# Optimization experiments

Measured on AMD Instinct MI355X. Metric: run time of the kernel, lower is better.

## Reference

```python
import jax, jax.numpy as jnp
import numpy as np

B, N, E, H = 2, 256, 768, 12
D = E // H
LOG_2PI = float(np.log(2.0 * np.pi))


def setup_inputs() -> dict:
    key = jax.random.key(0)
    ks = jax.random.split(key, 8)
    return {
        "x": jax.random.normal(ks[0], (B, N, E), jnp.float32),
        "Wqkv": jax.random.normal(ks[1], (E, 3 * E), jnp.float32) * 0.02,
        "bqkv": jax.random.normal(ks[2], (3 * E,), jnp.float32) * 0.02,
        "Wproj": jax.random.normal(ks[3], (E, E), jnp.float32) * 0.02,
        "bproj": jax.random.normal(ks[4], (E,), jnp.float32) * 0.02,
        "mean": jax.random.normal(ks[5], (E, E), jnp.float32),
        "logvar": jax.random.normal(ks[6], (E, E), jnp.float32),
        "mix_coef": jax.random.normal(ks[7], (E,), jnp.float32),
    }


def reference(x, Wqkv, bqkv, Wproj, bproj, mean, logvar, mix_coef):
    b, n, e = x.shape
    # qkv projection; einops 'b n (h d qkv) -> qkv b h n d' (qkv is the INNERMOST split)
    qkv = (x @ Wqkv + bqkv).reshape(b, n, H, D, 3)
    qkv = jnp.transpose(qkv, (4, 0, 2, 1, 3))  # (3, b, h, n, d)
    q, k, v = qkv[0], qkv[1], qkv[2]

    # keys back to (b, n, e): 'b h n d -> b n (h d)'
    keys = jnp.transpose(k, (0, 2, 1, 3)).reshape(b, n, e)

    # MixtureSameFamily.log_prob: component Normal batch (E, E), mixture over last dim.
    # out[b,n,i] = logsumexp_j( log_softmax(mix_coef)[j] + logN(keys[b,n,i]; mean[i,j], std[i,j]) )
    log_mix = jax.nn.log_softmax(mix_coef)                      # (E,)
    std = jnp.exp(0.5 * logvar)                                  # (E, E)
    z = (keys[:, :, :, None] - mean[None, None, :, :]) / std     # (b, n, E, E)
    comp_lp = -0.5 * (z * z) - jnp.log(std) - 0.5 * LOG_2PI      # (b, n, E, E)
    key_mix = jax.nn.logsumexp(comp_lp + log_mix, axis=-1)       # (b, n, E)

    # 'b n (h d) -> b h n d'
    key_mix = jnp.transpose(key_mix.reshape(b, n, H, D), (0, 2, 1, 3))

    energy = jnp.einsum("bhqd,bhkd->bhqk", q, key_mix)
    att = jax.nn.softmax(energy, axis=-1) / jnp.sqrt(jnp.float32(e))
    out = jnp.einsum("bhql,bhld->bhqd", att, v)                  # (b, h, n, d)
    out = jnp.transpose(out, (0, 2, 1, 3)).reshape(b, n, e)
    return out @ Wproj + bproj
```

## Files before the change

### kernel.cpp

```cpp
#include <hip/hip_runtime.h>

#define LOG2E 1.4426950408889634f
#define LN2 0.6931471805599453f

typedef __attribute__((ext_vector_type(8))) short bf16x8;
typedef __attribute__((ext_vector_type(4))) float f32x4;
typedef __attribute__((ext_vector_type(2))) float f32x2;

constexpr int Ee = 768;
constexpr int BN = 512;
constexpr long QC_OFF = 0;
constexpr long KT_OFF = 393216;
constexpr long VC_OFF = 786432;
constexpr long KM_OFF = 1179648;
constexpr long EN_OFF = 1572864;
constexpr long OA_OFF = 3145728;

__device__ __forceinline__ unsigned pk_hi(float x0, float x1) {
    return (__float_as_uint(x0) >> 16) | (__float_as_uint(x1) & 0xFFFF0000u);
}
__device__ __forceinline__ float rhi(float x) {
    return __uint_as_float(__float_as_uint(x) & 0xFFFF0000u);
}
__device__ __forceinline__ f32x2 pk_fma2(f32x2 a, f32x2 b, f32x2 c) {
    f32x2 d;
    asm("v_pk_fma_f32 %0, %1, %2, %3" : "=v"(d) : "v"(a), "v"(b), "v"(c));
    return d;
}
__device__ __forceinline__ f32x2 pk_add2(f32x2 a, f32x2 b) {
    f32x2 d;
    asm("v_pk_add_f32 %0, %1, %2" : "=v"(d) : "v"(a), "v"(b));
    return d;
}

template<int EPI>
__global__ __launch_bounds__(256)
void mfma_gemm(const float* __restrict__ A, int lda, long sAb, long sAh,
               const float* __restrict__ Bm, int ldb, long sBb, long sBh,
               float* __restrict__ C, int ldc, long sCb, long sCh,
               const float* __restrict__ bias, int K, int Hdiv,
               float* __restrict__ eq, float* __restrict__ ek,
               float* __restrict__ ev)
{
    __shared__ __align__(16) unsigned short sm[4 * 64 * 64];
    char* const smb = (char*)sm;
    const int tid = threadIdx.x;
    const int m0 = blockIdx.x * 64, n0 = blockIdx.y * 64;
    const int zb = blockIdx.z / Hdiv, zh = blockIdx.z - zb * Hdiv;
    A  += zb * sAb + zh * sAh;
    Bm += zb * sBb + zh * sBh;
    C  += zb * sCb + zh * sCh;

    const int lane = tid & 63, w = tid >> 6;
    const int wr = w >> 1, wc = w & 1;
    const int fr = lane & 15, fko2 = (lane >> 4) * 16;

    const bool isB = tid < 128;
    const int kq = isB ? (tid >> 4) : ((tid - 128) & 7);
    const int nq = tid & 15;
    const int mq = (tid - 128) >> 3;

    auto foff = [](int plane, int row, int cb) {
        return plane * 8192 + row * 128 + (cb ^ ((row & 7) << 4));
    };
    int wo[8];
    if (isB) {
        #pragma unroll
        for (int e = 0; e < 4; ++e) {
            wo[e]     = foff(2, nq * 4 + e, kq * 8);
            wo[e + 4] = foff(3, nq * 4 + e, kq * 8);
        }
    } else {
        #pragma unroll
        for (int r = 0; r < 4; ++r) {
            wo[r]     = foff(0, mq * 4 + r, kq * 8);
            wo[r + 4] = foff(1, mq * 4 + r, kq * 8);
        }
    }
    const int oA0h = foff(0, wr * 32 + fr,      fko2);
    const int oA1h = foff(0, wr * 32 + 16 + fr, fko2);
    const int oA0l = oA0h + 8192, oA1l = oA1h + 8192;
    const int oB0h = foff(2, wc * 32 + fr,      fko2);
    const int oB1h = foff(2, wc * 32 + 16 + fr, fko2);
    const int oB0l = oB0h + 8192, oB1l = oB1h + 8192;

    f32x4 acc00 = {}, acc01 = {}, acc10 = {}, acc11 = {};
    float4 r0, r1, r2, r3;

    auto load_regs = [&](int k0) {
        if (isB) {
            const float* p = &Bm[(long)(k0 + kq * 4) * ldb + n0 + nq * 4];
            r0 = *(const float4*)p; p += ldb;
            r1 = *(const float4*)p; p += ldb;
            r2 = *(const float4*)p; p += ldb;
            r3 = *(const float4*)p;
        } else {
            const float* p = &A[(long)(m0 + mq * 4) * lda + k0 + kq * 4];
            r0 = *(const float4*)p; p += lda;
            r1 = *(const float4*)p; p += lda;
            r2 = *(const float4*)p; p += lda;
            r3 = *(const float4*)p;
        }
    };

    auto cvt_store = [&](const float4& v, int o_hi, int o_lo) {
        uint2 hi; hi.x = pk_hi(v.x, v.y); hi.y = pk_hi(v.z, v.w);
        const float l0 = v.x - rhi(v.x), l1 = v.y - rhi(v.y);
        const float l2 = v.z - rhi(v.z), l3 = v.w - rhi(v.w);
        uint2 lo; lo.x = pk_hi(l0, l1); lo.y = pk_hi(l2, l3);
        *(uint2*)(smb + o_hi) = hi;
        *(uint2*)(smb + o_lo) = lo;
    };

    auto stage = [&]() {
        if (isB) {
            #pragma unroll
            for (int e = 0; e < 4; ++e) {
                float4 col;
                col.x = (&r0.x)[e]; col.y = (&r1.x)[e];
                col.z = (&r2.x)[e]; col.w = (&r3.x)[e];
                cvt_store(col, wo[e], wo[e + 4]);
            }
        } else {
            cvt_store(r0, wo[0], wo[4]);
            cvt_store(r1, wo[1], wo[5]);
            cvt_store(r2, wo[2], wo[6]);
            cvt_store(r3, wo[3], wo[7]);
        }
    };

    load_regs(0);
    for (int k0 = 0; k0 < K; k0 += 32) {
        __syncthreads();
        stage();
        __syncthreads();
        if (k0 + 32 < K) load_regs(k0 + 32);
        const bf16x8 Ah0 = *(const bf16x8*)(smb + oA0h);
        const bf16x8 Ah1 = *(const bf16x8*)(smb + oA1h);
        const bf16x8 Al0 = *(const bf16x8*)(smb + oA0l);
        const bf16x8 Al1 = *(const bf16x8*)(smb + oA1l);
        const bf16x8 Bh0 = *(const bf16x8*)(smb + oB0h);
        const bf16x8 Bh1 = *(const bf16x8*)(smb + oB1h);
        const bf16x8 Bl0 = *(const bf16x8*)(smb + oB0l);
        const bf16x8 Bl1 = *(const bf16x8*)(smb + oB1l);
        acc00 = __builtin_amdgcn_mfma_f32_16x16x32_bf16(Ah0, Bh0, acc00, 0, 0, 0);
        acc01 = __builtin_amdgcn_mfma_f32_16x16x32_bf16(Ah0, Bh1, acc01, 0, 0, 0);
        acc10 = __builtin_amdgcn_mfma_f32_16x16x32_bf16(Ah1, Bh0, acc10, 0, 0, 0);
        acc11 = __builtin_amdgcn_mfma_f32_16x16x32_bf16(Ah1, Bh1, acc11, 0, 0, 0);
        acc00 = __builtin_amdgcn_mfma_f32_16x16x32_bf16(Ah0, Bl0, acc00, 0, 0, 0);
        acc01 = __builtin_amdgcn_mfma_f32_16x16x32_bf16(Ah0, Bl1, acc01, 0, 0, 0);
        acc10 = __builtin_amdgcn_mfma_f32_16x16x32_bf16(Ah1, Bl0, acc10, 0, 0, 0);
        acc11 = __builtin_amdgcn_mfma_f32_16x16x32_bf16(Ah1, Bl1, acc11, 0, 0, 0);
        acc00 = __builtin_amdgcn_mfma_f32_16x16x32_bf16(Al0, Bh0, acc00, 0, 0, 0);
        acc01 = __builtin_amdgcn_mfma_f32_16x16x32_bf16(Al0, Bh1, acc01, 0, 0, 0);
        acc10 = __builtin_amdgcn_mfma_f32_16x16x32_bf16(Al1, Bh0, acc10, 0, 0, 0);
        acc11 = __builtin_amdgcn_mfma_f32_16x16x32_bf16(Al1, Bh1, acc11, 0, 0, 0);
    }

    const int rb = m0 + wr * 32 + (lane >> 4) * 4;
    const int cb = n0 + wc * 32 + fr;
    if (EPI == 1) {
        auto scat = [&](int row, int col, float x) {
            x += bias[col];
            const int i = col / 3, s = col - i * 3;
            if (s == 0)      eq[(long)row * Ee + i] = x;
            else if (s == 1) ek[(long)i * BN + row] = x;
            else             ev[(long)row * Ee + i] = x;
        };
        #pragma unroll
        for (int j = 0; j < 4; ++j) {
            scat(rb + j,      cb,      acc00[j]);
            scat(rb + j,      cb + 16, acc01[j]);
            scat(rb + j + 16, cb,      acc10[j]);
            scat(rb + j + 16, cb + 16, acc11[j]);
        }
    } else {
        const float b0  = bias ? bias[cb]      : 0.f;
        const float b16 = bias ? bias[cb + 16] : 0.f;
        #pragma unroll
        for (int j = 0; j < 4; ++j) C[(long)(rb + j +  0) * ldc + cb +  0] = acc00[j] + b0;
        #pragma unroll
        for (int j = 0; j < 4; ++j) C[(long)(rb + j +  0) * ldc + cb + 16] = acc01[j] + b16;
        #pragma unroll
        for (int j = 0; j < 4; ++j) C[(long)(rb + j + 16) * ldc + cb +  0] = acc10[j] + b0;
        #pragma unroll
        for (int j = 0; j < 4; ++j) C[(long)(rb + j + 16) * ldc + cb + 16] = acc11[j] + b16;
    }
}

__global__ __launch_bounds__(512)
void k_mixture(const float* __restrict__ mean, const float* __restrict__ logvar,
               const float* __restrict__ mix, const float* __restrict__ keysT,
               float* __restrict__ kmT)
{
    __shared__ __align__(16) float aS[768], bS[768], cS[768];
    __shared__ float sP[512][9];
    const int i = blockIdx.x;
    const int tid = threadIdx.x;

    for (int j = tid; j < 768; j += 512) {
        const float lv = logvar[i * Ee + j];
        const float mu = mean[i * Ee + j];
        const float istd2 = __builtin_amdgcn_exp2f(-lv * LOG2E);
        aS[j] = -0.5f * LOG2E * istd2;
        bS[j] = LOG2E * mu * istd2;
        cS[j] = fmaf(-0.5f * LOG2E * mu * mu, istd2, LOG2E * (mix[j] - 0.5f * lv));
    }
    __syncthreads();

    const int rg = tid & 63;
    const int jg = tid >> 6;
    f32x2 kvd[8], k2d[8], s2[8];
    #pragma unroll
    for (int q = 0; q < 8; ++q) {
        const float kv = keysT[(long)i * BN + q * 64 + rg];
        const float k2 = kv * kv;
        kvd[q] = (f32x2){kv, kv};
        k2d[q] = (f32x2){k2, k2};
        s2[q] = (f32x2){0.f, 0.f};
    }
    const float4* a4 = (const float4*)(aS + jg * 96);
    const float4* b4 = (const float4*)(bS + jg * 96);
    const float4* c4 = (const float4*)(cS + jg * 96);
    for (int it = 0; it < 24; ++it) {
        const float4 a = a4[it], b = b4[it], c = c4[it];
        const f32x2 a01 = {a.x, a.y}, a23 = {a.z, a.w};
        const f32x2 b01 = {b.x, b.y}, b23 = {b.z, b.w};
        const f32x2 c01 = {c.x, c.y}, c23 = {c.z, c.w};
        #pragma unroll
        for (int q = 0; q < 8; ++q) {
            f32x2 t0 = pk_fma2(a01, k2d[q], pk_fma2(b01, kvd[q], c01));
            f32x2 t1 = pk_fma2(a23, k2d[q], pk_fma2(b23, kvd[q], c23));
            f32x2 e0 = { __builtin_amdgcn_exp2f(t0.x), __builtin_amdgcn_exp2f(t0.y) };
            f32x2 e1 = { __builtin_amdgcn_exp2f(t1.x), __builtin_amdgcn_exp2f(t1.y) };
            s2[q] = pk_add2(s2[q], e0);
            s2[q] = pk_add2(s2[q], e1);
        }
    }
    #pragma unroll
    for (int q = 0; q < 8; ++q)
        sP[q * 64 + rg][jg] = s2[q].x + s2[q].y;
    __syncthreads();

    const float* rp = sP[tid];
    const float t0 = ((rp[0] + rp[1]) + (rp[2] + rp[3]))
                   + ((rp[4] + rp[5]) + (rp[6] + rp[7]));
    kmT[(long)i * BN + tid] = LN2 * __builtin_amdgcn_logf(t0);
}

__global__ __launch_bounds__(256)
void k_smpv(const float* __restrict__ energy, const float* __restrict__ vc,
            float* __restrict__ oat)
{
    __shared__ __align__(16) unsigned short att[32768];
    __shared__ __align__(16) unsigned short bv[8192];
    char* const attb = (char*)att;
    char* const bvb  = (char*)bv;
    const int tid = threadIdx.x;
    const int tile = blockIdx.x, bh = blockIdx.y;
    const int b = bh / 12, h = bh - b * 12;
    const float* E = energy + (long)bh * 65536 + (long)tile * 64 * 256;
    const float* V = vc + (long)b * 196608 + h * 64;
    float* O = oat + ((long)b * 256 + tile * 64) * 768 + h * 64;

    const int w = tid >> 6, lane = tid & 63;

    {
        const int rl = w * 16 + (lane >> 2);
        const int mq = (lane & 3) * 64;
        float4 ev[16];
        const float* erow = E + (long)rl * 256 + mq;
        #pragma unroll
        for (int t = 0; t < 16; ++t) ev[t] = *(const float4*)(erow + t * 4);
        float mx = -__builtin_inff();
        #pragma unroll
        for (int t = 0; t < 16; ++t)
            mx = fmaxf(mx, fmaxf(fmaxf(ev[t].x, ev[t].y), fmaxf(ev[t].z, ev[t].w)));
        mx = fmaxf(mx, __shfl_xor(mx, 1, 64));
        mx = fmaxf(mx, __shfl_xor(mx, 2, 64));
        float sum = 0.f;
        #pragma unroll
        for (int t = 0; t < 16; ++t) {
            ev[t].x = __builtin_amdgcn_exp2f((ev[t].x - mx) * LOG2E);
            ev[t].y = __builtin_amdgcn_exp2f((ev[t].y - mx) * LOG2E);
            ev[t].z = __builtin_amdgcn_exp2f((ev[t].z - mx) * LOG2E);
            ev[t].w = __builtin_amdgcn_exp2f((ev[t].w - mx) * LOG2E);
            sum += (ev[t].x + ev[t].y) + (ev[t].z + ev[t].w);
        }
        sum += __shfl_xor(sum, 1, 64);
        sum += __shfl_xor(sum, 2, 64);
        const float sc = 1.0f / (sum * 27.712812921102035f);
        const int rxor = (rl & 7) << 4;
        #pragma unroll
        for (int t = 0; t < 16; ++t) {
            const float x0 = ev[t].x * sc, x1 = ev[t].y * sc;
            const float x2 = ev[t].z * sc, x3 = ev[t].w * sc;
            uint2 hi; hi.x = pk_hi(x0, x1); hi.y = pk_hi(x2, x3);
            const float l0 = x0 - rhi(x0), l1 = x1 - rhi(x1);
            const float l2 = x2 - rhi(x2), l3 = x3 - rhi(x3);
            uint2 lo; lo.x = pk_hi(l0, l1); lo.y = pk_hi(l2, l3);
            const int cb = (mq + t * 4) * 2;
            *(uint2*)(attb + (long)rl * 512 + (cb ^ rxor))         = hi;
            *(uint2*)(attb + 32768 + (long)rl * 512 + (cb ^ rxor)) = lo;
        }
    }

    const int wr = w >> 1, wc = w & 1;
    const int fr = lane & 15, fko2 = (lane >> 4) * 16;
    const int rA0 = wr * 32 + fr, rA1 = rA0 + 16;
    const int rB0 = wc * 32 + fr, rB1 = rB0 + 16;
    const int xA0 = (rA0 & 7) << 4, xA1 = (rA1 & 7) << 4;
    const int oB0h = rB0 * 128 + (fko2 ^ ((rB0 & 7) << 4));
    const int oB1h = rB1 * 128 + (fko2 ^ ((rB1 & 7) << 4));
    const int oB0l = oB0h + 8192, oB1l = oB1h + 8192;

    const bool isB = tid < 128;
    const int kq = tid >> 4;
    const int nq = tid & 15;
    int wo[8];
    #pragma unroll
    for (int e = 0; e < 4; ++e) {
        const int row = nq * 4 + e;
        wo[e]     = row * 128 + ((kq * 8) ^ ((row & 7) << 4));
        wo[e + 4] = wo[e] + 8192;
    }

    f32x4 acc00 = {}, acc01 = {}, acc10 = {}, acc11 = {};
    float4 r0, r1, r2, r3;
    auto load_regs = [&](int k0) {
        if (isB) {
            const float* p = &V[(long)(k0 + kq * 4) * 768 + nq * 4];
            r0 = *(const float4*)p; p += 768;
            r1 = *(const float4*)p; p += 768;
            r2 = *(const float4*)p; p += 768;
            r3 = *(const float4*)p;
        }
    };
    auto cvt_store = [&](const float4& v, int o_hi, int o_lo) {
        uint2 hi; hi.x = pk_hi(v.x, v.y); hi.y = pk_hi(v.z, v.w);
        const float l0 = v.x - rhi(v.x), l1 = v.y - rhi(v.y);
        const float l2 = v.z - rhi(v.z), l3 = v.w - rhi(v.w);
        uint2 lo; lo.x = pk_hi(l0, l1); lo.y = pk_hi(l2, l3);
        *(uint2*)(bvb + o_hi) = hi;
        *(uint2*)(bvb + o_lo) = lo;
    };

    load_regs(0);
    for (int k0 = 0; k0 < 256; k0 += 32) {
        __syncthreads();
        if (isB) {
            #pragma unroll
            for (int e = 0; e < 4; ++e) {
                float4 col;
                col.x = (&r0.x)[e]; col.y = (&r1.x)[e];
                col.z = (&r2.x)[e]; col.w = (&r3.x)[e];
                cvt_store(col, wo[e], wo[e + 4]);
            }
        }
        __syncthreads();
        if (k0 + 32 < 256) load_regs(k0 + 32);
        const int cA = k0 * 2 + fko2;
        const bf16x8 Ah0 = *(const bf16x8*)(attb + (long)rA0 * 512 + (cA ^ xA0));
        const bf16x8 Ah1 = *(const bf16x8*)(attb + (long)rA1 * 512 + (cA ^ xA1));
        const bf16x8 Al0 = *(const bf16x8*)(attb + 32768 + (long)rA0 * 512 + (cA ^ xA0));
        const bf16x8 Al1 = *(const bf16x8*)(attb + 32768 + (long)rA1 * 512 + (cA ^ xA1));
        const bf16x8 Bh0 = *(const bf16x8*)(bvb + oB0h);
        const bf16x8 Bh1 = *(const bf16x8*)(bvb + oB1h);
        const bf16x8 Bl0 = *(const bf16x8*)(bvb + oB0l);
        const bf16x8 Bl1 = *(const bf16x8*)(bvb + oB1l);
        acc00 = __builtin_amdgcn_mfma_f32_16x16x32_bf16(Ah0, Bh0, acc00, 0, 0, 0);
        acc01 = __builtin_amdgcn_mfma_f32_16x16x32_bf16(Ah0, Bh1, acc01, 0, 0, 0);
        acc10 = __builtin_amdgcn_mfma_f32_16x16x32_bf16(Ah1, Bh0, acc10, 0, 0, 0);
        acc11 = __builtin_amdgcn_mfma_f32_16x16x32_bf16(Ah1, Bh1, acc11, 0, 0, 0);
        acc00 = __builtin_amdgcn_mfma_f32_16x16x32_bf16(Ah0, Bl0, acc00, 0, 0, 0);
        acc01 = __builtin_amdgcn_mfma_f32_16x16x32_bf16(Ah0, Bl1, acc01, 0, 0, 0);
        acc10 = __builtin_amdgcn_mfma_f32_16x16x32_bf16(Ah1, Bl0, acc10, 0, 0, 0);
        acc11 = __builtin_amdgcn_mfma_f32_16x16x32_bf16(Ah1, Bl1, acc11, 0, 0, 0);
        acc00 = __builtin_amdgcn_mfma_f32_16x16x32_bf16(Al0, Bh0, acc00, 0, 0, 0);
        acc01 = __builtin_amdgcn_mfma_f32_16x16x32_bf16(Al0, Bh1, acc01, 0, 0, 0);
        acc10 = __builtin_amdgcn_mfma_f32_16x16x32_bf16(Al1, Bh0, acc10, 0, 0, 0);
        acc11 = __builtin_amdgcn_mfma_f32_16x16x32_bf16(Al1, Bh1, acc11, 0, 0, 0);
    }

    const int rb = wr * 32 + (lane >> 4) * 4;
    const int cb = wc * 32 + fr;
    #pragma unroll
    for (int j = 0; j < 4; ++j) O[(long)(rb + j +  0) * 768 + cb +  0] = acc00[j];
    #pragma unroll
    for (int j = 0; j < 4; ++j) O[(long)(rb + j +  0) * 768 + cb + 16] = acc01[j];
    #pragma unroll
    for (int j = 0; j < 4; ++j) O[(long)(rb + j + 16) * 768 + cb +  0] = acc10[j];
    #pragma unroll
    for (int j = 0; j < 4; ++j) O[(long)(rb + j + 16) * 768 + cb + 16] = acc11[j];
}

extern "C" void kernel_launch(void* const* d_in, const int* in_sizes, int n_in,
                              void* d_out, int out_size, void* d_ws, size_t ws_size,
                              hipStream_t stream)
{
    (void)in_sizes; (void)n_in; (void)out_size; (void)ws_size;
    const float* x      = (const float*)d_in[0];
    const float* Wqkv   = (const float*)d_in[1];
    const float* bqkv   = (const float*)d_in[2];
    const float* Wproj  = (const float*)d_in[3];
    const float* bproj  = (const float*)d_in[4];
    const float* mean   = (const float*)d_in[5];
    const float* logvar = (const float*)d_in[6];
    const float* mixc   = (const float*)d_in[7];
    float* out = (float*)d_out;
    float* ws = (float*)d_ws;
    float* qc     = ws + QC_OFF;
    float* keysT  = ws + KT_OFF;
    float* vc     = ws + VC_OFF;
    float* kmT    = ws + KM_OFF;
    float* energy = ws + EN_OFF;
    float* oat    = ws + OA_OFF;

    mfma_gemm<1><<<dim3(8,36,1),256,0,stream>>>(
        x,768,0,0, Wqkv,2304,0,0, nullptr,0,0,0, bqkv, 768, 1,
        qc, keysT, vc);
    k_mixture<<<768,512,0,stream>>>(mean, logvar, mixc, keysT, kmT);
    mfma_gemm<0><<<dim3(4,4,24),256,0,stream>>>(
        qc,768,196608,64, kmT,512,256,32768, energy,256,786432,65536,
        nullptr, 64, 12, nullptr,nullptr,nullptr);
    k_smpv<<<dim3(4,24,1),256,0,stream>>>(energy, vc, oat);
    mfma_gemm<0><<<dim3(8,12,1),256,0,stream>>>(
        oat,768,0,0, Wproj,768,0,0, out,768,0,0, bproj, 768, 1,
        nullptr,nullptr,nullptr);
}
```

Baseline: 102.5 us.

## Fuse QK^T energy GEMM into softmax-PV attention kernel

The separate energy GEMM launch and its global energy buffer are removed. The new attention kernel computes the 64x256 score tile per block in MFMA accumulators, then does softmax with cross-wave reductions through shared memory. It writes the split bf16 attention into LDS and runs the PV product there. This removes one kernel launch and an energy round trip through global memory. In exchange, only 96 blocks do the QK work, where the old GEMM used 384, and register pressure rises with 64 accumulator floats per lane.

```diff
diff --git a/kernel.cpp b/kernel.cpp
--- a/kernel.cpp
+++ b/kernel.cpp
@@ -13,8 +13,7 @@
 constexpr long KT_OFF = 393216;
 constexpr long VC_OFF = 786432;
 constexpr long KM_OFF = 1179648;
-constexpr long EN_OFF = 1572864;
-constexpr long OA_OFF = 3145728;
+constexpr long OA_OFF = 1572864;
 
 __device__ __forceinline__ unsigned pk_hi(float x0, float x1) {
     return (__float_as_uint(x0) >> 16) | (__float_as_uint(x1) & 0xFFFF0000u);
@@ -249,94 +248,244 @@
 }
 
 __global__ __launch_bounds__(256)
-void k_smpv(const float* __restrict__ energy, const float* __restrict__ vc,
-            float* __restrict__ oat)
+void k_attn(const float* __restrict__ qc, const float* __restrict__ kmT,
+            const float* __restrict__ vc, float* __restrict__ oat)
 {
     __shared__ __align__(16) unsigned short att[32768];
-    __shared__ __align__(16) unsigned short bv[8192];
+    __shared__ __align__(16) unsigned short bvs[8192];
+    __shared__ float sRed[2][64];
+    char* const smb  = (char*)att;
     char* const attb = (char*)att;
-    char* const bvb  = (char*)bv;
+    char* const bvb  = (char*)bvs;
     const int tid = threadIdx.x;
     const int tile = blockIdx.x, bh = blockIdx.y;
     const int b = bh / 12, h = bh - b * 12;
-    const float* E = energy + (long)bh * 65536 + (long)tile * 64 * 256;
-    const float* V = vc + (long)b * 196608 + h * 64;
+    const float* Aq = qc  + ((long)b * 256 + tile * 64) * 768 + h * 64;
+    const float* Bk = kmT + (long)h * 64 * 512 + b * 256;
+    const float* V  = vc  + (long)b * 196608 + h * 64;
     float* O = oat + ((long)b * 256 + tile * 64) * 768 + h * 64;
 
-    const int w = tid >> 6, lane = tid & 63;
-
-    {
-        const int rl = w * 16 + (lane >> 2);
-        const int mq = (lane & 3) * 64;
-        float4 ev[16];
-        const float* erow = E + (long)rl * 256 + mq;
-        #pragma unroll
-        for (int t = 0; t < 16; ++t) ev[t] = *(const float4*)(erow + t * 4);
-        float mx = -__builtin_inff();
-        #pragma unroll
-        for (int t = 0; t < 16; ++t)
-            mx = fmaxf(mx, fmaxf(fmaxf(ev[t].x, ev[t].y), fmaxf(ev[t].z, ev[t].w)));
-        mx = fmaxf(mx, __shfl_xor(mx, 1, 64));
-        mx = fmaxf(mx, __shfl_xor(mx, 2, 64));
-        float sum = 0.f;
-        #pragma unroll
-        for (int t = 0; t < 16; ++t) {
-            ev[t].x = __builtin_amdgcn_exp2f((ev[t].x - mx) * LOG2E);
-            ev[t].y = __builtin_amdgcn_exp2f((ev[t].y - mx) * LOG2E);
-            ev[t].z = __builtin_amdgcn_exp2f((ev[t].z - mx) * LOG2E);
-            ev[t].w = __builtin_amdgcn_exp2f((ev[t].w - mx) * LOG2E);
-            sum += (ev[t].x + ev[t].y) + (ev[t].z + ev[t].w);
-        }
-        sum += __shfl_xor(sum, 1, 64);
-        sum += __shfl_xor(sum, 2, 64);
-        const float sc = 1.0f / (sum * 27.712812921102035f);
-        const int rxor = (rl & 7) << 4;
-        #pragma unroll
-        for (int t = 0; t < 16; ++t) {
-            const float x0 = ev[t].x * sc, x1 = ev[t].y * sc;
-            const float x2 = ev[t].z * sc, x3 = ev[t].w * sc;
-            uint2 hi; hi.x = pk_hi(x0, x1); hi.y = pk_hi(x2, x3);
-            const float l0 = x0 - rhi(x0), l1 = x1 - rhi(x1);
-            const float l2 = x2 - rhi(x2), l3 = x3 - rhi(x3);
-            uint2 lo; lo.x = pk_hi(l0, l1); lo.y = pk_hi(l2, l3);
-            const int cb = (mq + t * 4) * 2;
-            *(uint2*)(attb + (long)rl * 512 + (cb ^ rxor))         = hi;
-            *(uint2*)(attb + 32768 + (long)rl * 512 + (cb ^ rxor)) = lo;
-        }
-    }
-
+    const int lane = tid & 63, w = tid >> 6;
     const int wr = w >> 1, wc = w & 1;
     const int fr = lane & 15, fko2 = (lane >> 4) * 16;
-    const int rA0 = wr * 32 + fr, rA1 = rA0 + 16;
-    const int rB0 = wc * 32 + fr, rB1 = rB0 + 16;
-    const int xA0 = (rA0 & 7) << 4, xA1 = (rA1 & 7) << 4;
-    const int oB0h = rB0 * 128 + (fko2 ^ ((rB0 & 7) << 4));
-    const int oB1h = rB1 * 128 + (fko2 ^ ((rB1 & 7) << 4));
+    const bool isB = tid < 128;
+    const int kq = isB ? (tid >> 4) : ((tid - 128) & 7);
+    const int nq = tid & 15;
+    const int mq = (tid - 128) >> 3;
+
+    auto foff = [](int plane, int row, int cb) {
+        return plane * 8192 + row * 128 + (cb ^ ((row & 7) << 4));
+    };
+    int wo[8];
+    if (isB) {
+        #pragma unroll
+        for (int e = 0; e < 4; ++e) {
+            wo[e]     = foff(2, nq * 4 + e, kq * 8);
+            wo[e + 4] = foff(3, nq * 4 + e, kq * 8);
+        }
+    } else {
+        #pragma unroll
+        for (int r = 0; r < 4; ++r) {
+            wo[r]     = foff(0, mq * 4 + r, kq * 8);
+            wo[r + 4] = foff(1, mq * 4 + r, kq * 8);
+        }
+    }
+    const int oA0h = foff(0, wr * 32 + fr,      fko2);
+    const int oA1h = foff(0, wr * 32 + 16 + fr, fko2);
+    const int oA0l = oA0h + 8192, oA1l = oA1h + 8192;
+    const int oB0h = foff(2, wc * 32 + fr,      fko2);
+    const int oB1h = foff(2, wc * 32 + 16 + fr, fko2);
     const int oB0l = oB0h + 8192, oB1l = oB1h + 8192;
 
-    const bool isB = tid < 128;
-    const int kq = tid >> 4;
-    const int nq = tid & 15;
-    int wo[8];
-    #pragma unroll
-    for (int e = 0; e < 4; ++e) {
-        const int row = nq * 4 + e;
-        wo[e]     = row * 128 + ((kq * 8) ^ ((row & 7) << 4));
-        wo[e + 4] = wo[e] + 8192;
-    }
-
-    f32x4 acc00 = {}, acc01 = {}, acc10 = {}, acc11 = {};
     float4 r0, r1, r2, r3;
-    auto load_regs = [&](int k0) {
+    auto cvt_store = [&](const float4& v, int o_hi, int o_lo) {
+        uint2 hi; hi.x = pk_hi(v.x, v.y); hi.y = pk_hi(v.z, v.w);
+        const float l0 = v.x - rhi(v.x), l1 = v.y - rhi(v.y);
+        const float l2 = v.z - rhi(v.z), l3 = v.w - rhi(v.w);
+        uint2 lo; lo.x = pk_hi(l0, l1); lo.y = pk_hi(l2, l3);
+        *(uint2*)(smb + o_hi) = hi;
+        *(uint2*)(smb + o_lo) = lo;
+    };
+    auto stage = [&]() {
         if (isB) {
-            const float* p = &V[(long)(k0 + kq * 4) * 768 + nq * 4];
+            #pragma unroll
+            for (int e = 0; e < 4; ++e) {
+                float4 col;
+                col.x = (&r0.x)[e]; col.y = (&r1.x)[e];
+                col.z = (&r2.x)[e]; col.w = (&r3.x)[e];
+                cvt_store(col, wo[e], wo[e + 4]);
+            }
+        } else {
+            cvt_store(r0, wo[0], wo[4]);
+            cvt_store(r1, wo[1], wo[5]);
+            cvt_store(r2, wo[2], wo[6]);
+            cvt_store(r3, wo[3], wo[7]);
+        }
+    };
+
+    auto loadE = [&](int nt, int k0) {
+        if (isB) {
+            const float* p = &Bk[(long)(k0 + kq * 4) * 512 + nt * 64 + nq * 4];
+            r0 = *(const float4*)p; p += 512;
+            r1 = *(const float4*)p; p += 512;
+            r2 = *(const float4*)p; p += 512;
+            r3 = *(const float4*)p;
+        } else {
+            const float* p = &Aq[(long)(mq * 4) * 768 + k0 + kq * 4];
             r0 = *(const float4*)p; p += 768;
             r1 = *(const float4*)p; p += 768;
             r2 = *(const float4*)p; p += 768;
             r3 = *(const float4*)p;
         }
     };
-    auto cvt_store = [&](const float4& v, int o_hi, int o_lo) {
+
+    f32x4 accA[4][4] = {};
+    loadE(0, 0);
+    #pragma unroll
+    for (int step = 0; step < 8; ++step) {
+        const int nt = step >> 1;
+        __syncthreads();
+        stage();
+        __syncthreads();
+        if (step < 7) loadE((step + 1) >> 1, ((step + 1) & 1) * 32);
+        const bf16x8 Ah0 = *(const bf16x8*)(smb + oA0h);
+        const bf16x8 Ah1 = *(const bf16x8*)(smb + oA1h);
+        const bf16x8 Al0 = *(const bf16x8*)(smb + oA0l);
+        const bf16x8 Al1 = *(const bf16x8*)(smb + oA1l);
+        const bf16x8 Bh0 = *(const bf16x8*)(smb + oB0h);
+        const bf16x8 Bh1 = *(const bf16x8*)(smb + oB1h);
+        const bf16x8 Bl0 = *(const bf16x8*)(smb + oB0l);
+        const bf16x8 Bl1 = *(const bf16x8*)(smb + oB1l);
+        accA[nt][0] = __builtin_amdgcn_mfma_f32_16x16x32_bf16(Ah0, Bh0, accA[nt][0], 0, 0, 0);
+        accA[nt][1] = __builtin_amdgcn_mfma_f32_16x16x32_bf16(Ah0, Bh1, accA[nt][1], 0, 0, 0);
+        accA[nt][2] = __builtin_amdgcn_mfma_f32_16x16x32_bf16(Ah1, Bh0, accA[nt][2], 0, 0, 0);
+        accA[nt][3] = __builtin_amdgcn_mfma_f32_16x16x32_bf16(Ah1, Bh1, accA[nt][3], 0, 0, 0);
+        accA[nt][0] = __builtin_amdgcn_mfma_f32_16x16x32_bf16(Ah0, Bl0, accA[nt][0], 0, 0, 0);
+        accA[nt][1] = __builtin_amdgcn_mfma_f32_16x16x32_bf16(Ah0, Bl1, accA[nt][1], 0, 0, 0);
+        accA[nt][2] = __builtin_amdgcn_mfma_f32_16x16x32_bf16(Ah1, Bl0, accA[nt][2], 0, 0, 0);
+        accA[nt][3] = __builtin_amdgcn_mfma_f32_16x16x32_bf16(Ah1, Bl1, accA[nt][3], 0, 0, 0);
+        accA[nt][0] = __builtin_amdgcn_mfma_f32_16x16x32_bf16(Al0, Bh0, accA[nt][0], 0, 0, 0);
+        accA[nt][1] = __builtin_amdgcn_mfma_f32_16x16x32_bf16(Al0, Bh1, accA[nt][1], 0, 0, 0);
+        accA[nt][2] = __builtin_amdgcn_mfma_f32_16x16x32_bf16(Al1, Bh0, accA[nt][2], 0, 0, 0);
+        accA[nt][3] = __builtin_amdgcn_mfma_f32_16x16x32_bf16(Al1, Bh1, accA[nt][3], 0, 0, 0);
+    }
+
+    const int rbase = wr * 32 + (lane >> 4) * 4;
+    float mx0[4], mx1[4];
+    #pragma unroll
+    for (int j = 0; j < 4; ++j) {
+        float m0 = -__builtin_inff(), m1 = -__builtin_inff();
+        #pragma unroll
+        for (int nt = 0; nt < 4; ++nt) {
+            m0 = fmaxf(m0, fmaxf(accA[nt][0][j], accA[nt][1][j]));
+            m1 = fmaxf(m1, fmaxf(accA[nt][2][j], accA[nt][3][j]));
+        }
+        mx0[j] = m0; mx1[j] = m1;
+    }
+    #pragma unroll
+    for (int off = 1; off < 16; off <<= 1) {
+        #pragma unroll
+        for (int j = 0; j < 4; ++j) {
+            mx0[j] = fmaxf(mx0[j], __shfl_xor(mx0[j], off, 64));
+            mx1[j] = fmaxf(mx1[j], __shfl_xor(mx1[j], off, 64));
+        }
+    }
+    if (fr == 0) {
+        #pragma unroll
+        for (int j = 0; j < 4; ++j) {
+            sRed[wc][rbase + j]      = mx0[j];
+            sRed[wc][rbase + 16 + j] = mx1[j];
+        }
+    }
+    __syncthreads();
+    #pragma unroll
+    for (int j = 0; j < 4; ++j) {
+        mx0[j] = fmaxf(sRed[0][rbase + j],      sRed[1][rbase + j]);
+        mx1[j] = fmaxf(sRed[0][rbase + 16 + j], sRed[1][rbase + 16 + j]);
+    }
+    __syncthreads();
+    float s0[4] = {}, s1[4] = {};
+    #pragma unroll
+    for (int nt = 0; nt < 4; ++nt) {
+        #pragma unroll
+        for (int j = 0; j < 4; ++j) {
+            accA[nt][0][j] = __builtin_amdgcn_exp2f((accA[nt][0][j] - mx0[j]) * LOG2E);
+            accA[nt][1][j] = __builtin_amdgcn_exp2f((accA[nt][1][j] - mx0[j]) * LOG2E);
+            accA[nt][2][j] = __builtin_amdgcn_exp2f((accA[nt][2][j] - mx1[j]) * LOG2E);
+            accA[nt][3][j] = __builtin_amdgcn_exp2f((accA[nt][3][j] - mx1[j]) * LOG2E);
+            s0[j] += accA[nt][0][j] + accA[nt][1][j];
+            s1[j] += accA[nt][2][j] + accA[nt][3][j];
+        }
+    }
+    #pragma unroll
+    for (int off = 1; off < 16; off <<= 1) {
+        #pragma unroll
+        for (int j = 0; j < 4; ++j) {
+            s0[j] += __shfl_xor(s0[j], off, 64);
+            s1[j] += __shfl_xor(s1[j], off, 64);
+        }
+    }
+    if (fr == 0) {
+        #pragma unroll
+        for (int j = 0; j < 4; ++j) {
+            sRed[wc][rbase + j]      = s0[j];
+            sRed[wc][rbase + 16 + j] = s1[j];
+        }
+    }
+    __syncthreads();
+    float sc0[4], sc1[4];
+    #pragma unroll
+    for (int j = 0; j < 4; ++j) {
+        sc0[j] = 1.0f / ((sRed[0][rbase + j]      + sRed[1][rbase + j])      * 27.712812921102035f);
+        sc1[j] = 1.0f / ((sRed[0][rbase + 16 + j] + sRed[1][rbase + 16 + j]) * 27.712812921102035f);
+    }
+
+    const int kqV = tid >> 4;
+    int woV[8];
+    #pragma unroll
+    for (int e = 0; e < 4; ++e) {
+        const int row = nq * 4 + e;
+        woV[e]     = row * 128 + ((kqV * 8) ^ ((row & 7) << 4));
+        woV[e + 4] = woV[e] + 8192;
+    }
+    auto loadV = [&](int k0) {
+        if (isB) {
+            const float* p = &V[(long)(k0 + kqV * 4) * 768 + nq * 4];
+            r0 = *(const float4*)p; p += 768;
+            r1 = *(const float4*)p; p += 768;
+            r2 = *(const float4*)p; p += 768;
+            r3 = *(const float4*)p;
+        }
+    };
+    loadV(0);
+
+    auto wAtt = [&](int r, int c, float x) {
+        const int off = r * 512 + ((c * 2) ^ ((r & 7) << 4));
+        *(unsigned short*)(attb + off) = (unsigned short)(__float_as_uint(x) >> 16);
+        const float l = x - rhi(x);
+        *(unsigned short*)(attb + 32768 + off) = (unsigned short)(__float_as_uint(l) >> 16);
+    };
+    #pragma unroll
+    for (int nt = 0; nt < 4; ++nt) {
+        const int c0 = nt * 64 + wc * 32 + fr;
+        #pragma unroll
+        for (int j = 0; j < 4; ++j) {
+            wAtt(rbase + j,      c0,      accA[nt][0][j] * sc0[j]);
+            wAtt(rbase + j,      c0 + 16, accA[nt][1][j] * sc0[j]);
+            wAtt(rbase + 16 + j, c0,      accA[nt][2][j] * sc1[j]);
+            wAtt(rbase + 16 + j, c0 + 16, accA[nt][3][j] * sc1[j]);
+        }
+    }
+
+    const int rA0 = wr * 32 + fr, rA1 = rA0 + 16;
+    const int xA0 = (rA0 & 7) << 4, xA1 = (rA1 & 7) << 4;
+    const int rB0 = wc * 32 + fr, rB1 = rB0 + 16;
+    const int oV0h = rB0 * 128 + (fko2 ^ ((rB0 & 7) << 4));
+    const int oV1h = rB1 * 128 + (fko2 ^ ((rB1 & 7) << 4));
+    const int oV0l = oV0h + 8192, oV1l = oV1h + 8192;
+
+    f32x4 acc00 = {}, acc01 = {}, acc10 = {}, acc11 = {};
+    auto cvt_storeV = [&](const float4& v, int o_hi, int o_lo) {
         uint2 hi; hi.x = pk_hi(v.x, v.y); hi.y = pk_hi(v.z, v.w);
         const float l0 = v.x - rhi(v.x), l1 = v.y - rhi(v.y);
         const float l2 = v.z - rhi(v.z), l3 = v.w - rhi(v.w);
@@ -344,8 +493,6 @@
         *(uint2*)(bvb + o_hi) = hi;
         *(uint2*)(bvb + o_lo) = lo;
     };
-
-    load_regs(0);
     for (int k0 = 0; k0 < 256; k0 += 32) {
         __syncthreads();
         if (isB) {
@@ -354,20 +501,20 @@
                 float4 col;
                 col.x = (&r0.x)[e]; col.y = (&r1.x)[e];
                 col.z = (&r2.x)[e]; col.w = (&r3.x)[e];
-                cvt_store(col, wo[e], wo[e + 4]);
+                cvt_storeV(col, woV[e], woV[e + 4]);
             }
         }
         __syncthreads();
-        if (k0 + 32 < 256) load_regs(k0 + 32);
+        if (k0 + 32 < 256) loadV(k0 + 32);
         const int cA = k0 * 2 + fko2;
         const bf16x8 Ah0 = *(const bf16x8*)(attb + (long)rA0 * 512 + (cA ^ xA0));
         const bf16x8 Ah1 = *(const bf16x8*)(attb + (long)rA1 * 512 + (cA ^ xA1));
         const bf16x8 Al0 = *(const bf16x8*)(attb + 32768 + (long)rA0 * 512 + (cA ^ xA0));
         const bf16x8 Al1 = *(const bf16x8*)(attb + 32768 + (long)rA1 * 512 + (cA ^ xA1));
-        const bf16x8 Bh0 = *(const bf16x8*)(bvb + oB0h);
-        const bf16x8 Bh1 = *(const bf16x8*)(bvb + oB1h);
-        const bf16x8 Bl0 = *(const bf16x8*)(bvb + oB0l);
-        const bf16x8 Bl1 = *(const bf16x8*)(bvb + oB1l);
+        const bf16x8 Bh0 = *(const bf16x8*)(bvb + oV0h);
+        const bf16x8 Bh1 = *(const bf16x8*)(bvb + oV1h);
+        const bf16x8 Bl0 = *(const bf16x8*)(bvb + oV0l);
+        const bf16x8 Bl1 = *(const bf16x8*)(bvb + oV1l);
         acc00 = __builtin_amdgcn_mfma_f32_16x16x32_bf16(Ah0, Bh0, acc00, 0, 0, 0);
         acc01 = __builtin_amdgcn_mfma_f32_16x16x32_bf16(Ah0, Bh1, acc01, 0, 0, 0);
         acc10 = __builtin_amdgcn_mfma_f32_16x16x32_bf16(Ah1, Bh0, acc10, 0, 0, 0);
@@ -413,17 +560,13 @@
     float* keysT  = ws + KT_OFF;
     float* vc     = ws + VC_OFF;
     float* kmT    = ws + KM_OFF;
-    float* energy = ws + EN_OFF;
     float* oat    = ws + OA_OFF;
 
     mfma_gemm<1><<<dim3(8,36,1),256,0,stream>>>(
         x,768,0,0, Wqkv,2304,0,0, nullptr,0,0,0, bqkv, 768, 1,
         qc, keysT, vc);
     k_mixture<<<768,512,0,stream>>>(mean, logvar, mixc, keysT, kmT);
-    mfma_gemm<0><<<dim3(4,4,24),256,0,stream>>>(
-        qc,768,196608,64, kmT,512,256,32768, energy,256,786432,65536,
-        nullptr, 64, 12, nullptr,nullptr,nullptr);
-    k_smpv<<<dim3(4,24,1),256,0,stream>>>(energy, vc, oat);
+    k_attn<<<dim3(4,24,1),256,0,stream>>>(qc, kmT, vc, oat);
     mfma_gemm<0><<<dim3(8,12,1),256,0,stream>>>(
         oat,768,0,0, Wproj,768,0,0, out,768,0,0, bproj, 768, 1,
         nullptr,nullptr,nullptr);
```

Measured after the change: 106.5 us. 3.9% more time.

## Double-buffer LDS tiles in GEMM and softmax-PV kernels to drop a barrier

Applied to the files above, without the earlier changes.

Both the generic MFMA GEMM and the softmax·V kernel now ping-pong between two LDS buffers. The next tile is staged into the alternate buffer after the MFMAs, so only one __syncthreads per k-step remains instead of two. In k_smpv the first V tile load is also hoisted ahead of the softmax phase so its global latency overlaps that work. The cost is double the LDS for these buffers, which may lower occupancy, especially in k_smpv where the attention tile is already large.

```diff
diff --git a/kernel.cpp b/kernel.cpp
--- a/kernel.cpp
+++ b/kernel.cpp
@@ -42,7 +42,7 @@
                float* __restrict__ eq, float* __restrict__ ek,
                float* __restrict__ ev)
 {
-    __shared__ __align__(16) unsigned short sm[4 * 64 * 64];
+    __shared__ __align__(16) unsigned short sm[2 * 4 * 64 * 64];
     char* const smb = (char*)sm;
     const int tid = threadIdx.x;
     const int m0 = blockIdx.x * 64, n0 = blockIdx.y * 64;
@@ -112,37 +112,38 @@
         *(uint2*)(smb + o_lo) = lo;
     };
 
-    auto stage = [&]() {
+    auto stage = [&](int bo) {
         if (isB) {
             #pragma unroll
             for (int e = 0; e < 4; ++e) {
                 float4 col;
                 col.x = (&r0.x)[e]; col.y = (&r1.x)[e];
                 col.z = (&r2.x)[e]; col.w = (&r3.x)[e];
-                cvt_store(col, wo[e], wo[e + 4]);
+                cvt_store(col, bo + wo[e], bo + wo[e + 4]);
             }
         } else {
-            cvt_store(r0, wo[0], wo[4]);
-            cvt_store(r1, wo[1], wo[5]);
-            cvt_store(r2, wo[2], wo[6]);
-            cvt_store(r3, wo[3], wo[7]);
+            cvt_store(r0, bo + wo[0], bo + wo[4]);
+            cvt_store(r1, bo + wo[1], bo + wo[5]);
+            cvt_store(r2, bo + wo[2], bo + wo[6]);
+            cvt_store(r3, bo + wo[3], bo + wo[7]);
         }
     };
 
     load_regs(0);
+    stage(0);
+    __syncthreads();
+    int bo = 0;
     for (int k0 = 0; k0 < K; k0 += 32) {
-        __syncthreads();
-        stage();
-        __syncthreads();
-        if (k0 + 32 < K) load_regs(k0 + 32);
-        const bf16x8 Ah0 = *(const bf16x8*)(smb + oA0h);
-        const bf16x8 Ah1 = *(const bf16x8*)(smb + oA1h);
-        const bf16x8 Al0 = *(const bf16x8*)(smb + oA0l);
-        const bf16x8 Al1 = *(const bf16x8*)(smb + oA1l);
-        const bf16x8 Bh0 = *(const bf16x8*)(smb + oB0h);
-        const bf16x8 Bh1 = *(const bf16x8*)(smb + oB1h);
-        const bf16x8 Bl0 = *(const bf16x8*)(smb + oB0l);
-        const bf16x8 Bl1 = *(const bf16x8*)(smb + oB1l);
+        const bool more = (k0 + 32 < K);
+        if (more) load_regs(k0 + 32);
+        const bf16x8 Ah0 = *(const bf16x8*)(smb + bo + oA0h);
+        const bf16x8 Ah1 = *(const bf16x8*)(smb + bo + oA1h);
+        const bf16x8 Al0 = *(const bf16x8*)(smb + bo + oA0l);
+        const bf16x8 Al1 = *(const bf16x8*)(smb + bo + oA1l);
+        const bf16x8 Bh0 = *(const bf16x8*)(smb + bo + oB0h);
+        const bf16x8 Bh1 = *(const bf16x8*)(smb + bo + oB1h);
+        const bf16x8 Bl0 = *(const bf16x8*)(smb + bo + oB0l);
+        const bf16x8 Bl1 = *(const bf16x8*)(smb + bo + oB1l);
         acc00 = __builtin_amdgcn_mfma_f32_16x16x32_bf16(Ah0, Bh0, acc00, 0, 0, 0);
         acc01 = __builtin_amdgcn_mfma_f32_16x16x32_bf16(Ah0, Bh1, acc01, 0, 0, 0);
         acc10 = __builtin_amdgcn_mfma_f32_16x16x32_bf16(Ah1, Bh0, acc10, 0, 0, 0);
@@ -155,6 +156,9 @@
         acc01 = __builtin_amdgcn_mfma_f32_16x16x32_bf16(Al0, Bh1, acc01, 0, 0, 0);
         acc10 = __builtin_amdgcn_mfma_f32_16x16x32_bf16(Al1, Bh0, acc10, 0, 0, 0);
         acc11 = __builtin_amdgcn_mfma_f32_16x16x32_bf16(Al1, Bh1, acc11, 0, 0, 0);
+        if (more) stage(bo ^ 32768);
+        __syncthreads();
+        bo ^= 32768;
     }
 
     const int rb = m0 + wr * 32 + (lane >> 4) * 4;
@@ -253,9 +257,9 @@
             float* __restrict__ oat)
 {
     __shared__ __align__(16) unsigned short att[32768];
-    __shared__ __align__(16) unsigned short bv[8192];
+    __shared__ __align__(16) unsigned short bvs[16384];
     char* const attb = (char*)att;
-    char* const bvb  = (char*)bv;
+    char* const bvb  = (char*)bvs;
     const int tid = threadIdx.x;
     const int tile = blockIdx.x, bh = blockIdx.y;
     const int b = bh / 12, h = bh - b * 12;
@@ -264,6 +268,21 @@
     float* O = oat + ((long)b * 256 + tile * 64) * 768 + h * 64;
 
     const int w = tid >> 6, lane = tid & 63;
+    const bool isB = tid < 128;
+    const int kq = tid >> 4;
+    const int nq = tid & 15;
+
+    float4 r0, r1, r2, r3;
+    auto loadV = [&](int k0) {
+        if (isB) {
+            const float* p = &V[(long)(k0 + kq * 4) * 768 + nq * 4];
+            r0 = *(const float4*)p; p += 768;
+            r1 = *(const float4*)p; p += 768;
+            r2 = *(const float4*)p; p += 768;
+            r3 = *(const float4*)p;
+        }
+    };
+    loadV(0);
 
     {
         const int rl = w * 16 + (lane >> 2);
@@ -314,9 +333,6 @@
     const int oB1h = rB1 * 128 + (fko2 ^ ((rB1 & 7) << 4));
     const int oB0l = oB0h + 8192, oB1l = oB1h + 8192;
 
-    const bool isB = tid < 128;
-    const int kq = tid >> 4;
-    const int nq = tid & 15;
     int wo[8];
     #pragma unroll
     for (int e = 0; e < 4; ++e) {
@@ -324,50 +340,40 @@
         wo[e]     = row * 128 + ((kq * 8) ^ ((row & 7) << 4));
         wo[e + 4] = wo[e] + 8192;
     }
-
-    f32x4 acc00 = {}, acc01 = {}, acc10 = {}, acc11 = {};
-    float4 r0, r1, r2, r3;
-    auto load_regs = [&](int k0) {
-        if (isB) {
-            const float* p = &V[(long)(k0 + kq * 4) * 768 + nq * 4];
-            r0 = *(const float4*)p; p += 768;
-            r1 = *(const float4*)p; p += 768;
-            r2 = *(const float4*)p; p += 768;
-            r3 = *(const float4*)p;
-        }
-    };
-    auto cvt_store = [&](const float4& v, int o_hi, int o_lo) {
-        uint2 hi; hi.x = pk_hi(v.x, v.y); hi.y = pk_hi(v.z, v.w);
-        const float l0 = v.x - rhi(v.x), l1 = v.y - rhi(v.y);
-        const float l2 = v.z - rhi(v.z), l3 = v.w - rhi(v.w);
-        uint2 lo; lo.x = pk_hi(l0, l1); lo.y = pk_hi(l2, l3);
-        *(uint2*)(bvb + o_hi) = hi;
-        *(uint2*)(bvb + o_lo) = lo;
-    };
-
-    load_regs(0);
-    for (int k0 = 0; k0 < 256; k0 += 32) {
-        __syncthreads();
+    auto stageV = [&](int bo) {
         if (isB) {
             #pragma unroll
             for (int e = 0; e < 4; ++e) {
                 float4 col;
                 col.x = (&r0.x)[e]; col.y = (&r1.x)[e];
                 col.z = (&r2.x)[e]; col.w = (&r3.x)[e];
-                cvt_store(col, wo[e], wo[e + 4]);
+                const float4 v = col;
+                uint2 hi; hi.x = pk_hi(v.x, v.y); hi.y = pk_hi(v.z, v.w);
+                const float l0 = v.x - rhi(v.x), l1 = v.y - rhi(v.y);
+                const float l2 = v.z - rhi(v.z), l3 = v.w - rhi(v.w);
+                uint2 lo; lo.x = pk_hi(l0, l1); lo.y = pk_hi(l2, l3);
+                *(uint2*)(bvb + bo + wo[e])     = hi;
+                *(uint2*)(bvb + bo + wo[e + 4]) = lo;
             }
         }
-        __syncthreads();
-        if (k0 + 32 < 256) load_regs(k0 + 32);
+    };
+
+    f32x4 acc00 = {}, acc01 = {}, acc10 = {}, acc11 = {};
+    stageV(0);
+    __syncthreads();
+    int bo = 0;
+    for (int k0 = 0; k0 < 256; k0 += 32) {
+        const bool more = (k0 + 32 < 256);
+        if (more) loadV(k0 + 32);
         const int cA = k0 * 2 + fko2;
         const bf16x8 Ah0 = *(const bf16x8*)(attb + (long)rA0 * 512 + (cA ^ xA0));
         const bf16x8 Ah1 = *(const bf16x8*)(attb + (long)rA1 * 512 + (cA ^ xA1));
         const bf16x8 Al0 = *(const bf16x8*)(attb + 32768 + (long)rA0 * 512 + (cA ^ xA0));
         const bf16x8 Al1 = *(const bf16x8*)(attb + 32768 + (long)rA1 * 512 + (cA ^ xA1));
-        const bf16x8 Bh0 = *(const bf16x8*)(bvb + oB0h);
-        const bf16x8 Bh1 = *(const bf16x8*)(bvb + oB1h);
-        const bf16x8 Bl0 = *(const bf16x8*)(bvb + oB0l);
-        const bf16x8 Bl1 = *(const bf16x8*)(bvb + oB1l);
+        const bf16x8 Bh0 = *(const bf16x8*)(bvb + bo + oB0h);
+        const bf16x8 Bh1 = *(const bf16x8*)(bvb + bo + oB1h);
+        const bf16x8 Bl0 = *(const bf16x8*)(bvb + bo + oB0l);
+        const bf16x8 Bl1 = *(const bf16x8*)(bvb + bo + oB1l);
         acc00 = __builtin_amdgcn_mfma_f32_16x16x32_bf16(Ah0, Bh0, acc00, 0, 0, 0);
         acc01 = __builtin_amdgcn_mfma_f32_16x16x32_bf16(Ah0, Bh1, acc01, 0, 0, 0);
         acc10 = __builtin_amdgcn_mfma_f32_16x16x32_bf16(Ah1, Bh0, acc10, 0, 0, 0);
@@ -380,6 +386,9 @@
         acc01 = __builtin_amdgcn_mfma_f32_16x16x32_bf16(Al0, Bh1, acc01, 0, 0, 0);
         acc10 = __builtin_amdgcn_mfma_f32_16x16x32_bf16(Al1, Bh0, acc10, 0, 0, 0);
         acc11 = __builtin_amdgcn_mfma_f32_16x16x32_bf16(Al1, Bh1, acc11, 0, 0, 0);
+        if (more) stageV(bo ^ 16384);
+        __syncthreads();
+        bo ^= 16384;
     }
 
     const int rb = wr * 32 + (lane >> 4) * 4;
```

After: 113.5 us. 10.8% more time.
